# Performance work log

Hardware: AMD Instinct MI355X
Metric: run time of the kernel (lower is better)

## Reference

```python
import jax, jax.numpy as jnp
import numpy as np

DIM = 512
HEADS = 8
HEAD_DIM = DIM // HEADS
HIDDEN = 4 * DIM
EPS = 1e-5


def _ln(x, g, b):
    mu = jnp.mean(x, axis=-1, keepdims=True)
    var = jnp.mean((x - mu) ** 2, axis=-1, keepdims=True)
    return (x - mu) * jax.lax.rsqrt(var + EPS) * g + b


def setup_inputs() -> dict:
    key = jax.random.key(0)
    ks = jax.random.split(key, 12)
    s = lambda fan: 1.0 / np.sqrt(fan)
    return {
        "x": jax.random.normal(ks[0], (2, 4096, DIM), jnp.float32),
        "ln1_g": jnp.ones((DIM,), jnp.float32),
        "ln1_b": jnp.zeros((DIM,), jnp.float32),
        "ln2_g": jnp.ones((DIM,), jnp.float32),
        "ln2_b": jnp.zeros((DIM,), jnp.float32),
        "qkv_w": jax.random.normal(ks[1], (3 * DIM, DIM), jnp.float32) * s(DIM),
        "qkv_b": jnp.zeros((3 * DIM,), jnp.float32),
        "proj_w": jax.random.normal(ks[2], (DIM, DIM), jnp.float32) * s(DIM),
        "proj_b": jnp.zeros((DIM,), jnp.float32),
        "fc1_w": jax.random.normal(ks[3], (HIDDEN, DIM), jnp.float32) * s(DIM),
        "fc1_b": jnp.zeros((HIDDEN,), jnp.float32),
        "fc2_w": jax.random.normal(ks[4], (DIM, HIDDEN), jnp.float32) * s(HIDDEN),
        "fc2_b": jnp.zeros((DIM,), jnp.float32),
    }


def reference(x, ln1_g, ln1_b, ln2_g, ln2_b, qkv_w, qkv_b, proj_w, proj_b,
              fc1_w, fc1_b, fc2_w, fc2_b):
    B, N, C = x.shape
    # --- attention (pre-norm) ---
    h = _ln(x, ln1_g, ln1_b)
    qkv = h @ qkv_w.T + qkv_b                      # [B,N,3C]
    qkv = qkv.reshape(B, N, 3, HEADS, HEAD_DIM)
    q, k, v = (jnp.moveaxis(qkv, 2, 0)[i].transpose(0, 2, 1, 3) for i in range(3))  # [B,H,N,D]
    scale = HEAD_DIM ** -0.5
    attn = jax.nn.softmax(jnp.einsum('bhnd,bhmd->bhnm', q, k) * scale, axis=-1)
    out = jnp.einsum('bhnm,bhmd->bhnd', attn, v)   # [B,H,N,D]
    out = out.transpose(0, 2, 1, 3).reshape(B, N, C)
    x = x + out @ proj_w.T + proj_b
    # --- MLP (pre-norm) ---
    h = _ln(x, ln2_g, ln2_b)
    h = jax.nn.gelu(h @ fc1_w.T + fc1_b, approximate=False)
    return x + h @ fc2_w.T + fc2_b
```

## Files before the change

kernel.cpp:

```cpp
#include <hip/hip_runtime.h>
#include <hip/hip_bf16.h>
#include <hip/hip_fp16.h>
#include <string.h>

using bf16 = __hip_bfloat16;
typedef __attribute__((ext_vector_type(8))) short short8;
typedef __attribute__((ext_vector_type(8))) _Float16 half8;
typedef __attribute__((ext_vector_type(4))) float f32x4;
typedef __attribute__((ext_vector_type(16))) float f32x16;

#define GAS __attribute__((address_space(1)))
#define LAS __attribute__((address_space(3)))

__device__ __forceinline__ void gld_lds16(const void* g, void* l) {
  __builtin_amdgcn_global_load_lds((const GAS void*)g, (LAS void*)l, 16, 0, 0);
}

__device__ __forceinline__ unsigned short f2bfu(float f) {
  bf16 h = __float2bfloat16(f);
  return *reinterpret_cast<unsigned short*>(&h);
}

__device__ __forceinline__ unsigned pack_bf16x2(float lo, float hi) {
  __hip_bfloat162 v = __float22bfloat162_rn(make_float2(lo, hi));
  unsigned u;
  __builtin_memcpy(&u, &v, 4);
  return u;
}

__device__ __forceinline__ unsigned pack_f16x2(float lo, float hi) {
  __half2 v = __float22half2_rn(make_float2(lo, hi));
  unsigned u;
  __builtin_memcpy(&u, &v, 4);
  return u;
}

__global__ __launch_bounds__(256) void cvt_all(const float* __restrict__ w0, bf16* __restrict__ o0,
                                               const float* __restrict__ w1, bf16* __restrict__ o1,
                                               const float* __restrict__ w2, bf16* __restrict__ o2,
                                               const float* __restrict__ w3, bf16* __restrict__ o3) {
  int i = blockIdx.x * 256 + threadIdx.x;
  const float* src; bf16* dst; int off;
  if (i < 196608)      { src = w0; dst = o0; off = i; }
  else if (i < 262144) { src = w1; dst = o1; off = i - 196608; }
  else if (i < 524288) { src = w2; dst = o2; off = i - 262144; }
  else                 { src = w3; dst = o3; off = i - 524288; }
  float4 v = reinterpret_cast<const float4*>(src)[off];
  ushort4 o;
  o.x = f2bfu(v.x); o.y = f2bfu(v.y); o.z = f2bfu(v.z); o.w = f2bfu(v.w);
  reinterpret_cast<ushort4*>(dst)[off] = o;
}

__global__ __launch_bounds__(256) void ln_kernel(const float* __restrict__ x,
                                                 const float* __restrict__ g,
                                                 const float* __restrict__ b,
                                                 bf16* __restrict__ out) {
  const int row = blockIdx.x * 4 + (threadIdx.x >> 6);
  const int lane = threadIdx.x & 63;
  const float4* xr = reinterpret_cast<const float4*>(x + (size_t)row * 512);
  float4 v0 = xr[lane], v1 = xr[64 + lane];
  float s  = v0.x + v0.y + v0.z + v0.w + v1.x + v1.y + v1.z + v1.w;
  float s2 = v0.x*v0.x + v0.y*v0.y + v0.z*v0.z + v0.w*v0.w
           + v1.x*v1.x + v1.y*v1.y + v1.z*v1.z + v1.w*v1.w;
  #pragma unroll
  for (int d = 1; d < 64; d <<= 1) { s += __shfl_xor(s, d); s2 += __shfl_xor(s2, d); }
  const float mu = s * (1.0f / 512.0f);
  const float var = s2 * (1.0f / 512.0f) - mu * mu;
  const float rstd = rsqrtf(var + 1e-5f);
  const float4* g4 = reinterpret_cast<const float4*>(g);
  const float4* b4 = reinterpret_cast<const float4*>(b);
  float4 ga = g4[lane], gb = g4[64 + lane], ba = b4[lane], bb = b4[64 + lane];
  ushort4 o0, o1;
  o0.x = f2bfu((v0.x - mu) * rstd * ga.x + ba.x);
  o0.y = f2bfu((v0.y - mu) * rstd * ga.y + ba.y);
  o0.z = f2bfu((v0.z - mu) * rstd * ga.z + ba.z);
  o0.w = f2bfu((v0.w - mu) * rstd * ga.w + ba.w);
  o1.x = f2bfu((v1.x - mu) * rstd * gb.x + bb.x);
  o1.y = f2bfu((v1.y - mu) * rstd * gb.y + bb.y);
  o1.z = f2bfu((v1.z - mu) * rstd * gb.z + bb.z);
  o1.w = f2bfu((v1.w - mu) * rstd * gb.w + bb.w);
  ushort4* orow = reinterpret_cast<ushort4*>(out + (size_t)row * 512);
  orow[lane] = o0;
  orow[64 + lane] = o1;
}

template <int EPI>
__global__ __launch_bounds__(256) void gemm_bt(const bf16* __restrict__ A,
                                               const bf16* __restrict__ B,
                                               const float* __restrict__ bias,
                                               const float* __restrict__ resid,
                                               void* __restrict__ Cv,
                                               int M, int N, int K) {
  __shared__ bf16 As[128 * 32];
  __shared__ bf16 Bs[128 * 32];
  const int tid = threadIdx.x;
  const int lane = tid & 63, wid = tid >> 6;
  const int lr = lane & 15, lg = lane >> 4;
  const int row0 = blockIdx.x * 128, col0 = blockIdx.y * 128;
  const int wr = (wid >> 1) * 64, wc = (wid & 1) * 64;
  f32x4 acc[4][4] = {};
  const int r1 = tid >> 2,          c1 = (tid & 3) * 8;
  const int r2 = (256 + tid) >> 2,  c2 = ((256 + tid) & 3) * 8;
  for (int kt = 0; kt < K; kt += 32) {
    __syncthreads();
    gld_lds16(A + (size_t)(row0 + r1) * K + kt + c1, As + tid * 8);
    gld_lds16(A + (size_t)(row0 + r2) * K + kt + c2, As + (256 + tid) * 8);
    gld_lds16(B + (size_t)(col0 + r1) * K + kt + c1, Bs + tid * 8);
    gld_lds16(B + (size_t)(col0 + r2) * K + kt + c2, Bs + (256 + tid) * 8);
    __syncthreads();
    short8 af[4], bfr[4];
    #pragma unroll
    for (int mi = 0; mi < 4; ++mi)
      af[mi] = *reinterpret_cast<const short8*>(&As[(wr + mi * 16 + lr) * 32 + lg * 8]);
    #pragma unroll
    for (int nj = 0; nj < 4; ++nj)
      bfr[nj] = *reinterpret_cast<const short8*>(&Bs[(wc + nj * 16 + lr) * 32 + lg * 8]);
    #pragma unroll
    for (int mi = 0; mi < 4; ++mi)
      #pragma unroll
      for (int nj = 0; nj < 4; ++nj)
        acc[mi][nj] = __builtin_amdgcn_mfma_f32_16x16x32_bf16(af[mi], bfr[nj], acc[mi][nj], 0, 0, 0);
  }
  #pragma unroll
  for (int mi = 0; mi < 4; ++mi) {
    #pragma unroll
    for (int nj = 0; nj < 4; ++nj) {
      const int col = col0 + wc + nj * 16 + lr;
      const float bv = bias ? bias[col] : 0.0f;
      #pragma unroll
      for (int rg = 0; rg < 4; ++rg) {
        const int row = row0 + wr + mi * 16 + lg * 4 + rg;
        float v = acc[mi][nj][rg] + bv;
        if constexpr (EPI == 1) v = 0.5f * v * (1.0f + erff(v * 0.70710678118654752f));
        if constexpr (EPI == 2) {
          reinterpret_cast<float*>(Cv)[(size_t)row * N + col] = v + resid[(size_t)row * N + col];
        } else if constexpr (EPI == 3) {
          reinterpret_cast<__half*>(Cv)[(size_t)row * N + col] = __float2half(v);
        } else {
          reinterpret_cast<bf16*>(Cv)[(size_t)row * N + col] = __float2bfloat16(v);
        }
      }
    }
  }
}

template <int EPI>
__global__ __launch_bounds__(256) void gemm_bt64(const bf16* __restrict__ A,
                                                 const bf16* __restrict__ B,
                                                 const float* __restrict__ bias,
                                                 const float* __restrict__ resid,
                                                 void* __restrict__ Cv,
                                                 int M, int N, int K) {
  __shared__ bf16 As[64 * 64];
  __shared__ bf16 Bs[64 * 64];
  const int tid = threadIdx.x;
  const int lane = tid & 63, wid = tid >> 6;
  const int lr = lane & 15, lg = lane >> 4;
  const int row0 = blockIdx.x * 64, col0 = blockIdx.y * 64;
  const int wr = (wid >> 1) * 32, wc = (wid & 1) * 32;
  f32x4 acc[2][2] = {};
  const int xsw = (lr & 7) << 4;
  const int fb0 = lr * 128 + ((lg * 16) ^ xsw);
  const int fb1 = lr * 128 + ((64 + lg * 16) ^ xsw);
  const int ph0 = tid * 16, ph1 = (256 + tid) * 16;
  const int r0 = ph0 >> 7, r1 = ph1 >> 7;
  const int lb0 = ph0 ^ ((r0 & 7) << 4), lb1 = ph1 ^ ((r1 & 7) << 4);
  const char* Ab0 = (const char*)A + (size_t)(row0 + r0) * K * 2 + (lb0 & 127);
  const char* Ab1 = (const char*)A + (size_t)(row0 + r1) * K * 2 + (lb1 & 127);
  const char* Bb0 = (const char*)B + (size_t)(col0 + r0) * K * 2 + (lb0 & 127);
  const char* Bb1 = (const char*)B + (size_t)(col0 + r1) * K * 2 + (lb1 & 127);
  for (int kt = 0; kt < K; kt += 64) {
    __syncthreads();
    gld_lds16(Ab0 + kt * 2, (char*)As + ph0);
    gld_lds16(Ab1 + kt * 2, (char*)As + ph1);
    gld_lds16(Bb0 + kt * 2, (char*)Bs + ph0);
    gld_lds16(Bb1 + kt * 2, (char*)Bs + ph1);
    __syncthreads();
    short8 af0[2], af1[2], bf0[2], bf1[2];
    #pragma unroll
    for (int mi = 0; mi < 2; ++mi) {
      af0[mi] = *reinterpret_cast<const short8*>((const char*)As + (wr + mi * 16) * 128 + fb0);
      af1[mi] = *reinterpret_cast<const short8*>((const char*)As + (wr + mi * 16) * 128 + fb1);
    }
    #pragma unroll
    for (int nj = 0; nj < 2; ++nj) {
      bf0[nj] = *reinterpret_cast<const short8*>((const char*)Bs + (wc + nj * 16) * 128 + fb0);
      bf1[nj] = *reinterpret_cast<const short8*>((const char*)Bs + (wc + nj * 16) * 128 + fb1);
    }
    #pragma unroll
    for (int mi = 0; mi < 2; ++mi)
      #pragma unroll
      for (int nj = 0; nj < 2; ++nj) {
        acc[mi][nj] = __builtin_amdgcn_mfma_f32_16x16x32_bf16(af0[mi], bf0[nj], acc[mi][nj], 0, 0, 0);
        acc[mi][nj] = __builtin_amdgcn_mfma_f32_16x16x32_bf16(af1[mi], bf1[nj], acc[mi][nj], 0, 0, 0);
      }
  }
  #pragma unroll
  for (int mi = 0; mi < 2; ++mi) {
    #pragma unroll
    for (int nj = 0; nj < 2; ++nj) {
      const int col = col0 + wc + nj * 16 + lr;
      const float bv = bias ? bias[col] : 0.0f;
      #pragma unroll
      for (int rg = 0; rg < 4; ++rg) {
        const int row = row0 + wr + mi * 16 + lg * 4 + rg;
        float v = acc[mi][nj][rg] + bv;
        if constexpr (EPI == 1) v = 0.5f * v * (1.0f + erff(v * 0.70710678118654752f));
        if constexpr (EPI == 2) {
          reinterpret_cast<float*>(Cv)[(size_t)row * N + col] = v + resid[(size_t)row * N + col];
        } else {
          reinterpret_cast<bf16*>(Cv)[(size_t)row * N + col] = __float2bfloat16(v);
        }
      }
    }
  }
}

__global__ __launch_bounds__(256) void reshape_qkv(const __half* __restrict__ C,
                                                   __half* __restrict__ q,
                                                   __half* __restrict__ KF,
                                                   __half* __restrict__ VF) {
  const int nt = blockIdx.x;
  const int bh = blockIdx.y;
  const int b = bh >> 3, h = bh & 7;
  __shared__ alignas(16) __half vs[64][72];
  const int tid = threadIdx.x;
  const float qs = 0.125f * 1.44269504088896340736f;
  #pragma unroll
  for (int i = 0; i < 16; ++i) {
    const int idx = i * 256 + tid;
    const int rr = idx >> 6, c = idx & 63;
    const size_t crow = ((size_t)b * 4096 + nt * 64 + rr) * 1536;
    const size_t onb = ((size_t)bh * 4096 + nt * 64 + rr) * 64 + c;
    q[onb] = __float2half(__half2float(C[crow + h * 64 + c]) * qs);
    vs[c][rr] = C[crow + 1024 + h * 64 + c];
  }
  #pragma unroll
  for (int i = 0; i < 2; ++i) {
    const int s = i * 256 + tid;
    const int half_ = s >> 8, dc = (s >> 6) & 3, l = s & 63;
    const int l31 = l & 31, hi2 = l >> 5;
    const __half* src = C + ((size_t)b * 4096 + nt * 64 + half_ * 32 + l31) * 1536
                          + 512 + h * 64 + dc * 16 + hi2 * 8;
    __half* dst = KF + ((size_t)bh * 128 + nt * 2 + half_) * 2048 + dc * 512 + (size_t)l * 8;
    *reinterpret_cast<short8*>(dst) = *reinterpret_cast<const short8*>(src);
  }
  __syncthreads();
  #pragma unroll
  for (int i = 0; i < 2; ++i) {
    const int s = i * 256 + tid;
    const int half_ = (s >> 8) & 1, db = (s >> 7) & 1, c = (s >> 6) & 1, l = s & 63;
    const int d = db * 32 + (l & 31);
    const int n0 = half_ * 32 + c * 16 + ((l >> 5) << 2);
    const short4 lo = *reinterpret_cast<const short4*>(&vs[d][n0]);
    const short4 hi = *reinterpret_cast<const short4*>(&vs[d][n0 + 8]);
    short8 v;
    v[0] = lo.x; v[1] = lo.y; v[2] = lo.z; v[3] = lo.w;
    v[4] = hi.x; v[5] = hi.y; v[6] = hi.z; v[7] = hi.w;
    __half* dst = VF + ((size_t)bh * 128 + nt * 2 + half_) * 2048 + (db * 2 + c) * 512 + (size_t)l * 8;
    *reinterpret_cast<short8*>(dst) = v;
  }
}

__global__ __launch_bounds__(256, 4) void attn_kernel(const __half* __restrict__ Q,
                                                      const __half* __restrict__ KF,
                                                      const __half* __restrict__ VF,
                                                      bf16* __restrict__ Out) {
  const int qt = blockIdx.x;
  const int bh = blockIdx.y;
  const int b = bh >> 3, h = bh & 7;
  __shared__ alignas(16) char smem[17408];
  const int tid = threadIdx.x, w = tid >> 6, lane = tid & 63;
  const int qg = w >> 1, kvh = w & 1;
  const int l31 = lane & 31, hi = lane >> 5;

  const __half* qrow = Q + ((size_t)bh * 4096 + qt * 64 + qg * 32 + l31) * 64 + hi * 8;
  const half8 qf0 = *reinterpret_cast<const half8*>(qrow);
  const half8 qf1 = *reinterpret_cast<const half8*>(qrow + 16);
  const half8 qf2 = *reinterpret_cast<const half8*>(qrow + 32);
  const half8 qf3 = *reinterpret_cast<const half8*>(qrow + 48);

  const char* kfp = (const char*)KF + (size_t)bh * 524288 + (size_t)kvh * 262144 + lane * 16;
  const char* vfp = (const char*)VF + (size_t)bh * 524288 + (size_t)kvh * 262144 + lane * 16;

  f32x16 O0 = {}, O1 = {};
  float mrow = -1e30f, lrow = 0.0f;

  for (int t = 0; t < 64; ++t) {
    const half8 va00 = *reinterpret_cast<const half8*>(vfp);
    const half8 va01 = *reinterpret_cast<const half8*>(vfp + 1024);
    const half8 va10 = *reinterpret_cast<const half8*>(vfp + 2048);
    const half8 va11 = *reinterpret_cast<const half8*>(vfp + 3072);
    vfp += 4096;
    const half8 kf0 = *reinterpret_cast<const half8*>(kfp);
    const half8 kf1 = *reinterpret_cast<const half8*>(kfp + 1024);
    const half8 kf2 = *reinterpret_cast<const half8*>(kfp + 2048);
    const half8 kf3 = *reinterpret_cast<const half8*>(kfp + 3072);
    kfp += 4096;
    f32x16 S = {};
    __builtin_amdgcn_s_setprio(1);
    S = __builtin_amdgcn_mfma_f32_32x32x16_f16(kf0, qf0, S, 0, 0, 0);
    S = __builtin_amdgcn_mfma_f32_32x32x16_f16(kf1, qf1, S, 0, 0, 0);
    S = __builtin_amdgcn_mfma_f32_32x32x16_f16(kf2, qf2, S, 0, 0, 0);
    S = __builtin_amdgcn_mfma_f32_32x32x16_f16(kf3, qf3, S, 0, 0, 0);
    __builtin_amdgcn_s_setprio(0);
    float a0 = fmaxf(fmaxf(S[0], S[1]), fmaxf(S[2], S[3]));
    float a1 = fmaxf(fmaxf(S[4], S[5]), fmaxf(S[6], S[7]));
    float a2 = fmaxf(fmaxf(S[8], S[9]), fmaxf(S[10], S[11]));
    float a3 = fmaxf(fmaxf(S[12], S[13]), fmaxf(S[14], S[15]));
    float rmax = fmaxf(fmaxf(a0, a1), fmaxf(a2, a3));
    float ra = rmax, rb = rmax;
    asm volatile("v_permlane32_swap_b32 %0, %1" : "+v"(ra), "+v"(rb));
    rmax = fmaxf(ra, rb);
    if (!__all(rmax <= mrow + 8.0f)) {
      const float mnew = fmaxf(mrow, rmax);
      const float fsc = __builtin_amdgcn_exp2f(mrow - mnew);
      lrow *= fsc;
      #pragma unroll
      for (int i = 0; i < 16; ++i) { O0[i] *= fsc; O1[i] *= fsc; }
      mrow = mnew;
    }
    #pragma unroll
    for (int i = 0; i < 16; ++i) S[i] = __builtin_amdgcn_exp2f(S[i] - mrow);
    float s0 = (S[0] + S[1]) + (S[2] + S[3]);
    float s1 = (S[4] + S[5]) + (S[6] + S[7]);
    float s2 = (S[8] + S[9]) + (S[10] + S[11]);
    float s3 = (S[12] + S[13]) + (S[14] + S[15]);
    float rsum = (s0 + s1) + (s2 + s3);
    float sa = rsum, sb = rsum;
    asm volatile("v_permlane32_swap_b32 %0, %1" : "+v"(sa), "+v"(sb));
    lrow += sa + sb;
    union U8 { unsigned u[4]; half8 h8; } up0, up1;
    up0.u[0] = pack_f16x2(S[0], S[1]);   up0.u[1] = pack_f16x2(S[2], S[3]);
    up0.u[2] = pack_f16x2(S[4], S[5]);   up0.u[3] = pack_f16x2(S[6], S[7]);
    up1.u[0] = pack_f16x2(S[8], S[9]);   up1.u[1] = pack_f16x2(S[10], S[11]);
    up1.u[2] = pack_f16x2(S[12], S[13]); up1.u[3] = pack_f16x2(S[14], S[15]);
    __builtin_amdgcn_s_setprio(1);
    O0 = __builtin_amdgcn_mfma_f32_32x32x16_f16(va00, up0.h8, O0, 0, 0, 0);
    O0 = __builtin_amdgcn_mfma_f32_32x32x16_f16(va01, up1.h8, O0, 0, 0, 0);
    O1 = __builtin_amdgcn_mfma_f32_32x32x16_f16(va10, up0.h8, O1, 0, 0, 0);
    O1 = __builtin_amdgcn_mfma_f32_32x32x16_f16(va11, up1.h8, O1, 0, 0, 0);
    __builtin_amdgcn_s_setprio(0);
  }

  __syncthreads();
  float* area = reinterpret_cast<float*>(smem) + qg * 2176;
  if (kvh) {
    #pragma unroll
    for (int r = 0; r < 16; ++r) {
      area[r * 64 + lane] = O0[r];
      area[(16 + r) * 64 + lane] = O1[r];
    }
    area[2048 + lane] = mrow;
    area[2112 + lane] = lrow;
  }
  __syncthreads();
  if (!kvh) {
    const float mB = area[2048 + lane], lB = area[2112 + lane];
    const float mx = fmaxf(mrow, mB);
    const float fa = __builtin_amdgcn_exp2f(mrow - mx);
    const float fb = __builtin_amdgcn_exp2f(mB - mx);
    const float inv = 1.0f / (lrow * fa + lB * fb);
    const int qrow2 = qt * 64 + qg * 32 + l31;
    bf16* ob = Out + ((size_t)b * 4096 + qrow2) * 512 + h * 64 + hi * 4;
    #pragma unroll
    for (int db = 0; db < 2; ++db) {
      #pragma unroll
      for (int rq = 0; rq < 4; ++rq) {
        const int r = rq * 4;
        float v0 = ((db ? O1[r + 0] : O0[r + 0]) * fa + area[(db * 16 + r + 0) * 64 + lane] * fb) * inv;
        float v1 = ((db ? O1[r + 1] : O0[r + 1]) * fa + area[(db * 16 + r + 1) * 64 + lane] * fb) * inv;
        float v2 = ((db ? O1[r + 2] : O0[r + 2]) * fa + area[(db * 16 + r + 2) * 64 + lane] * fb) * inv;
        float v3 = ((db ? O1[r + 3] : O0[r + 3]) * fa + area[(db * 16 + r + 3) * 64 + lane] * fb) * inv;
        uint2 st;
        st.x = pack_bf16x2(v0, v1);
        st.y = pack_bf16x2(v2, v3);
        *reinterpret_cast<uint2*>(ob + db * 32 + rq * 8) = st;
      }
    }
  }
}

extern "C" void kernel_launch(void* const* d_in, const int* in_sizes, int n_in,
                              void* d_out, int out_size, void* d_ws, size_t ws_size,
                              hipStream_t stream) {
  const float* x      = (const float*)d_in[0];
  const float* ln1_g  = (const float*)d_in[1];
  const float* ln1_b  = (const float*)d_in[2];
  const float* ln2_g  = (const float*)d_in[3];
  const float* ln2_b  = (const float*)d_in[4];
  const float* qkv_w  = (const float*)d_in[5];
  const float* qkv_b  = (const float*)d_in[6];
  const float* proj_w = (const float*)d_in[7];
  const float* proj_b = (const float*)d_in[8];
  const float* fc1_w  = (const float*)d_in[9];
  const float* fc1_b  = (const float*)d_in[10];
  const float* fc2_w  = (const float*)d_in[11];
  const float* fc2_b  = (const float*)d_in[12];

  char* ws = (char*)d_ws;
  constexpr size_t o_qkvw = 0;
  constexpr size_t o_projw = 1572864;
  constexpr size_t o_fc1w  = 2097152;
  constexpr size_t o_fc2w  = 4194304;
  constexpr size_t o_h     = 6291456;
  constexpr size_t o_qkvC  = 14680064;
  constexpr size_t o_q     = 39845888;
  constexpr size_t o_k     = 48234496;
  constexpr size_t o_vt    = 56623104;
  constexpr size_t o_attn  = 65011712;
  constexpr size_t o_x2    = 73400320;
  constexpr size_t o_fc1o  = o_qkvC;
  constexpr size_t needed  = 90177536;
  if (ws_size < needed) return;

  bf16* qkvw_bf = (bf16*)(ws + o_qkvw);
  bf16* projw_bf = (bf16*)(ws + o_projw);
  bf16* fc1w_bf = (bf16*)(ws + o_fc1w);
  bf16* fc2w_bf = (bf16*)(ws + o_fc2w);
  bf16* h     = (bf16*)(ws + o_h);
  __half* qkvC = (__half*)(ws + o_qkvC);
  __half* q    = (__half*)(ws + o_q);
  __half* kf   = (__half*)(ws + o_k);
  __half* vf   = (__half*)(ws + o_vt);
  bf16* attn  = (bf16*)(ws + o_attn);
  float* x2   = (float*)(ws + o_x2);
  bf16* fc1o  = (bf16*)(ws + o_fc1o);
  float* out  = (float*)d_out;

  cvt_all<<<3072, 256, 0, stream>>>(qkv_w, qkvw_bf, proj_w, projw_bf, fc1_w, fc1w_bf, fc2_w, fc2w_bf);

  ln_kernel<<<2048, 256, 0, stream>>>(x, ln1_g, ln1_b, h);
  gemm_bt<3><<<dim3(64, 12), 256, 0, stream>>>(h, qkvw_bf, qkv_b, nullptr, qkvC, 8192, 1536, 512);
  reshape_qkv<<<dim3(64, 16), 256, 0, stream>>>(qkvC, q, kf, vf);
  attn_kernel<<<dim3(64, 16), 256, 0, stream>>>(q, kf, vf, attn);
  gemm_bt64<2><<<dim3(128, 8), 256, 0, stream>>>(attn, projw_bf, proj_b, x, x2, 8192, 512, 512);
  ln_kernel<<<2048, 256, 0, stream>>>(x2, ln2_g, ln2_b, h);
  gemm_bt<1><<<dim3(64, 16), 256, 0, stream>>>(h, fc1w_bf, fc1_b, nullptr, fc1o, 8192, 2048, 512);
  gemm_bt64<2><<<dim3(128, 8), 256, 0, stream>>>(fc1o, fc2w_bf, fc2_b, x2, out, 8192, 512, 2048);
}
```

Measured before the change: 251.2 us.

## Process two query sub-tiles per wave in attention to reuse K/V fragments

Each wave now computes scores and softmax for two 32-row query blocks against the same K/V fragments. This halves global K/V loads per query row and gives more independent MFMA chains to interleave. The block covers 128 queries, the grid shrinks to 32x16, and launch bounds drop to 2 blocks per CU to allow the doubled accumulator register use. The risks are fewer resident waves to hide load latency and fewer blocks in total.

Result: faster. 238.4 us (-5.1%).

```diff
diff --git a/kernel.cpp b/kernel.cpp
--- a/kernel.cpp
+++ b/kernel.cpp
@@ -262,7 +262,7 @@
   }
 }
 
-__global__ __launch_bounds__(256, 4) void attn_kernel(const __half* __restrict__ Q,
+__global__ __launch_bounds__(256, 2) void attn_kernel(const __half* __restrict__ Q,
                                                       const __half* __restrict__ KF,
                                                       const __half* __restrict__ VF,
                                                       bf16* __restrict__ Out) {
@@ -274,17 +274,20 @@
   const int qg = w >> 1, kvh = w & 1;
   const int l31 = lane & 31, hi = lane >> 5;
 
-  const __half* qrow = Q + ((size_t)bh * 4096 + qt * 64 + qg * 32 + l31) * 64 + hi * 8;
-  const half8 qf0 = *reinterpret_cast<const half8*>(qrow);
-  const half8 qf1 = *reinterpret_cast<const half8*>(qrow + 16);
-  const half8 qf2 = *reinterpret_cast<const half8*>(qrow + 32);
-  const half8 qf3 = *reinterpret_cast<const half8*>(qrow + 48);
+  const __half* qbase = Q + ((size_t)bh * 4096 + qt * 128 + qg * 64 + l31) * 64 + hi * 8;
+  half8 qf0[4], qf1[4];
+  #pragma unroll
+  for (int dc = 0; dc < 4; ++dc) {
+    qf0[dc] = *reinterpret_cast<const half8*>(qbase + dc * 16);
+    qf1[dc] = *reinterpret_cast<const half8*>(qbase + 2048 + dc * 16);
+  }
 
   const char* kfp = (const char*)KF + (size_t)bh * 524288 + (size_t)kvh * 262144 + lane * 16;
   const char* vfp = (const char*)VF + (size_t)bh * 524288 + (size_t)kvh * 262144 + lane * 16;
 
-  f32x16 O0 = {}, O1 = {};
-  float mrow = -1e30f, lrow = 0.0f;
+  f32x16 O00 = {}, O01 = {};
+  f32x16 O10 = {}, O11 = {};
+  float m0 = -1e30f, l0 = 0.0f, m1 = -1e30f, l1 = 0.0f;
 
   for (int t = 0; t < 64; ++t) {
     const half8 va00 = *reinterpret_cast<const half8*>(vfp);
@@ -297,85 +300,134 @@
     const half8 kf2 = *reinterpret_cast<const half8*>(kfp + 2048);
     const half8 kf3 = *reinterpret_cast<const half8*>(kfp + 3072);
     kfp += 4096;
-    f32x16 S = {};
+    f32x16 S0 = {}, S1 = {};
     __builtin_amdgcn_s_setprio(1);
-    S = __builtin_amdgcn_mfma_f32_32x32x16_f16(kf0, qf0, S, 0, 0, 0);
-    S = __builtin_amdgcn_mfma_f32_32x32x16_f16(kf1, qf1, S, 0, 0, 0);
-    S = __builtin_amdgcn_mfma_f32_32x32x16_f16(kf2, qf2, S, 0, 0, 0);
-    S = __builtin_amdgcn_mfma_f32_32x32x16_f16(kf3, qf3, S, 0, 0, 0);
+    S0 = __builtin_amdgcn_mfma_f32_32x32x16_f16(kf0, qf0[0], S0, 0, 0, 0);
+    S1 = __builtin_amdgcn_mfma_f32_32x32x16_f16(kf0, qf1[0], S1, 0, 0, 0);
+    S0 = __builtin_amdgcn_mfma_f32_32x32x16_f16(kf1, qf0[1], S0, 0, 0, 0);
+    S1 = __builtin_amdgcn_mfma_f32_32x32x16_f16(kf1, qf1[1], S1, 0, 0, 0);
+    S0 = __builtin_amdgcn_mfma_f32_32x32x16_f16(kf2, qf0[2], S0, 0, 0, 0);
+    S1 = __builtin_amdgcn_mfma_f32_32x32x16_f16(kf2, qf1[2], S1, 0, 0, 0);
+    S0 = __builtin_amdgcn_mfma_f32_32x32x16_f16(kf3, qf0[3], S0, 0, 0, 0);
+    S1 = __builtin_amdgcn_mfma_f32_32x32x16_f16(kf3, qf1[3], S1, 0, 0, 0);
     __builtin_amdgcn_s_setprio(0);
-    float a0 = fmaxf(fmaxf(S[0], S[1]), fmaxf(S[2], S[3]));
-    float a1 = fmaxf(fmaxf(S[4], S[5]), fmaxf(S[6], S[7]));
-    float a2 = fmaxf(fmaxf(S[8], S[9]), fmaxf(S[10], S[11]));
-    float a3 = fmaxf(fmaxf(S[12], S[13]), fmaxf(S[14], S[15]));
-    float rmax = fmaxf(fmaxf(a0, a1), fmaxf(a2, a3));
-    float ra = rmax, rb = rmax;
-    asm volatile("v_permlane32_swap_b32 %0, %1" : "+v"(ra), "+v"(rb));
-    rmax = fmaxf(ra, rb);
-    if (!__all(rmax <= mrow + 8.0f)) {
-      const float mnew = fmaxf(mrow, rmax);
-      const float fsc = __builtin_amdgcn_exp2f(mrow - mnew);
-      lrow *= fsc;
-      #pragma unroll
-      for (int i = 0; i < 16; ++i) { O0[i] *= fsc; O1[i] *= fsc; }
-      mrow = mnew;
-    }
-    #pragma unroll
-    for (int i = 0; i < 16; ++i) S[i] = __builtin_amdgcn_exp2f(S[i] - mrow);
-    float s0 = (S[0] + S[1]) + (S[2] + S[3]);
-    float s1 = (S[4] + S[5]) + (S[6] + S[7]);
-    float s2 = (S[8] + S[9]) + (S[10] + S[11]);
-    float s3 = (S[12] + S[13]) + (S[14] + S[15]);
-    float rsum = (s0 + s1) + (s2 + s3);
-    float sa = rsum, sb = rsum;
-    asm volatile("v_permlane32_swap_b32 %0, %1" : "+v"(sa), "+v"(sb));
-    lrow += sa + sb;
-    union U8 { unsigned u[4]; half8 h8; } up0, up1;
-    up0.u[0] = pack_f16x2(S[0], S[1]);   up0.u[1] = pack_f16x2(S[2], S[3]);
-    up0.u[2] = pack_f16x2(S[4], S[5]);   up0.u[3] = pack_f16x2(S[6], S[7]);
-    up1.u[0] = pack_f16x2(S[8], S[9]);   up1.u[1] = pack_f16x2(S[10], S[11]);
-    up1.u[2] = pack_f16x2(S[12], S[13]); up1.u[3] = pack_f16x2(S[14], S[15]);
+    union U8 { unsigned u[4]; half8 h8; } p00, p01, p10, p11;
+    {
+      float a0 = fmaxf(fmaxf(S0[0], S0[1]), fmaxf(S0[2], S0[3]));
+      float a1 = fmaxf(fmaxf(S0[4], S0[5]), fmaxf(S0[6], S0[7]));
+      float a2 = fmaxf(fmaxf(S0[8], S0[9]), fmaxf(S0[10], S0[11]));
+      float a3 = fmaxf(fmaxf(S0[12], S0[13]), fmaxf(S0[14], S0[15]));
+      float rmax = fmaxf(fmaxf(a0, a1), fmaxf(a2, a3));
+      float ra = rmax, rb = rmax;
+      asm volatile("v_permlane32_swap_b32 %0, %1" : "+v"(ra), "+v"(rb));
+      rmax = fmaxf(ra, rb);
+      if (!__all(rmax <= m0 + 8.0f)) {
+        const float mnew = fmaxf(m0, rmax);
+        const float fsc = __builtin_amdgcn_exp2f(m0 - mnew);
+        l0 *= fsc;
+        #pragma unroll
+        for (int i = 0; i < 16; ++i) { O00[i] *= fsc; O01[i] *= fsc; }
+        m0 = mnew;
+      }
+      #pragma unroll
+      for (int i = 0; i < 16; ++i) S0[i] = __builtin_amdgcn_exp2f(S0[i] - m0);
+      float s0 = (S0[0] + S0[1]) + (S0[2] + S0[3]);
+      float s1 = (S0[4] + S0[5]) + (S0[6] + S0[7]);
+      float s2 = (S0[8] + S0[9]) + (S0[10] + S0[11]);
+      float s3 = (S0[12] + S0[13]) + (S0[14] + S0[15]);
+      float rsum = (s0 + s1) + (s2 + s3);
+      float sa = rsum, sb = rsum;
+      asm volatile("v_permlane32_swap_b32 %0, %1" : "+v"(sa), "+v"(sb));
+      l0 += sa + sb;
+      p00.u[0] = pack_f16x2(S0[0], S0[1]);   p00.u[1] = pack_f16x2(S0[2], S0[3]);
+      p00.u[2] = pack_f16x2(S0[4], S0[5]);   p00.u[3] = pack_f16x2(S0[6], S0[7]);
+      p01.u[0] = pack_f16x2(S0[8], S0[9]);   p01.u[1] = pack_f16x2(S0[10], S0[11]);
+      p01.u[2] = pack_f16x2(S0[12], S0[13]); p01.u[3] = pack_f16x2(S0[14], S0[15]);
+    }
+    {
+      float a0 = fmaxf(fmaxf(S1[0], S1[1]), fmaxf(S1[2], S1[3]));
+      float a1 = fmaxf(fmaxf(S1[4], S1[5]), fmaxf(S1[6], S1[7]));
+      float a2 = fmaxf(fmaxf(S1[8], S1[9]), fmaxf(S1[10], S1[11]));
+      float a3 = fmaxf(fmaxf(S1[12], S1[13]), fmaxf(S1[14], S1[15]));
+      float rmax = fmaxf(fmaxf(a0, a1), fmaxf(a2, a3));
+      float ra = rmax, rb = rmax;
+      asm volatile("v_permlane32_swap_b32 %0, %1" : "+v"(ra), "+v"(rb));
+      rmax = fmaxf(ra, rb);
+      if (!__all(rmax <= m1 + 8.0f)) {
+        const float mnew = fmaxf(m1, rmax);
+        const float fsc = __builtin_amdgcn_exp2f(m1 - mnew);
+        l1 *= fsc;
+        #pragma unroll
+        for (int i = 0; i < 16; ++i) { O10[i] *= fsc; O11[i] *= fsc; }
+        m1 = mnew;
+      }
+      #pragma unroll
+      for (int i = 0; i < 16; ++i) S1[i] = __builtin_amdgcn_exp2f(S1[i] - m1);
+      float s0 = (S1[0] + S1[1]) + (S1[2] + S1[3]);
+      float s1 = (S1[4] + S1[5]) + (S1[6] + S1[7]);
+      float s2 = (S1[8] + S1[9]) + (S1[10] + S1[11]);
+      float s3 = (S1[12] + S1[13]) + (S1[14] + S1[15]);
+      float rsum = (s0 + s1) + (s2 + s3);
+      float sa = rsum, sb = rsum;
+      asm volatile("v_permlane32_swap_b32 %0, %1" : "+v"(sa), "+v"(sb));
+      l1 += sa + sb;
+      p10.u[0] = pack_f16x2(S1[0], S1[1]);   p10.u[1] = pack_f16x2(S1[2], S1[3]);
+      p10.u[2] = pack_f16x2(S1[4], S1[5]);   p10.u[3] = pack_f16x2(S1[6], S1[7]);
+      p11.u[0] = pack_f16x2(S1[8], S1[9]);   p11.u[1] = pack_f16x2(S1[10], S1[11]);
+      p11.u[2] = pack_f16x2(S1[12], S1[13]); p11.u[3] = pack_f16x2(S1[14], S1[15]);
+    }
     __builtin_amdgcn_s_setprio(1);
-    O0 = __builtin_amdgcn_mfma_f32_32x32x16_f16(va00, up0.h8, O0, 0, 0, 0);
-    O0 = __builtin_amdgcn_mfma_f32_32x32x16_f16(va01, up1.h8, O0, 0, 0, 0);
-    O1 = __builtin_amdgcn_mfma_f32_32x32x16_f16(va10, up0.h8, O1, 0, 0, 0);
-    O1 = __builtin_amdgcn_mfma_f32_32x32x16_f16(va11, up1.h8, O1, 0, 0, 0);
+    O00 = __builtin_amdgcn_mfma_f32_32x32x16_f16(va00, p00.h8, O00, 0, 0, 0);
+    O10 = __builtin_amdgcn_mfma_f32_32x32x16_f16(va00, p10.h8, O10, 0, 0, 0);
+    O00 = __builtin_amdgcn_mfma_f32_32x32x16_f16(va01, p01.h8, O00, 0, 0, 0);
+    O10 = __builtin_amdgcn_mfma_f32_32x32x16_f16(va01, p11.h8, O10, 0, 0, 0);
+    O01 = __builtin_amdgcn_mfma_f32_32x32x16_f16(va10, p00.h8, O01, 0, 0, 0);
+    O11 = __builtin_amdgcn_mfma_f32_32x32x16_f16(va10, p10.h8, O11, 0, 0, 0);
+    O01 = __builtin_amdgcn_mfma_f32_32x32x16_f16(va11, p01.h8, O01, 0, 0, 0);
+    O11 = __builtin_amdgcn_mfma_f32_32x32x16_f16(va11, p11.h8, O11, 0, 0, 0);
     __builtin_amdgcn_s_setprio(0);
   }
 
-  __syncthreads();
   float* area = reinterpret_cast<float*>(smem) + qg * 2176;
-  if (kvh) {
-    #pragma unroll
-    for (int r = 0; r < 16; ++r) {
-      area[r * 64 + lane] = O0[r];
-      area[(16 + r) * 64 + lane] = O1[r];
-    }
-    area[2048 + lane] = mrow;
-    area[2112 + lane] = lrow;
-  }
-  __syncthreads();
-  if (!kvh) {
-    const float mB = area[2048 + lane], lB = area[2112 + lane];
-    const float mx = fmaxf(mrow, mB);
-    const float fa = __builtin_amdgcn_exp2f(mrow - mx);
-    const float fb = __builtin_amdgcn_exp2f(mB - mx);
-    const float inv = 1.0f / (lrow * fa + lB * fb);
-    const int qrow2 = qt * 64 + qg * 32 + l31;
-    bf16* ob = Out + ((size_t)b * 4096 + qrow2) * 512 + h * 64 + hi * 4;
-    #pragma unroll
-    for (int db = 0; db < 2; ++db) {
-      #pragma unroll
-      for (int rq = 0; rq < 4; ++rq) {
-        const int r = rq * 4;
-        float v0 = ((db ? O1[r + 0] : O0[r + 0]) * fa + area[(db * 16 + r + 0) * 64 + lane] * fb) * inv;
-        float v1 = ((db ? O1[r + 1] : O0[r + 1]) * fa + area[(db * 16 + r + 1) * 64 + lane] * fb) * inv;
-        float v2 = ((db ? O1[r + 2] : O0[r + 2]) * fa + area[(db * 16 + r + 2) * 64 + lane] * fb) * inv;
-        float v3 = ((db ? O1[r + 3] : O0[r + 3]) * fa + area[(db * 16 + r + 3) * 64 + lane] * fb) * inv;
-        uint2 st;
-        st.x = pack_bf16x2(v0, v1);
-        st.y = pack_bf16x2(v2, v3);
-        *reinterpret_cast<uint2*>(ob + db * 32 + rq * 8) = st;
+  #pragma unroll
+  for (int qs = 0; qs < 2; ++qs) {
+    const f32x16& Pd0 = qs ? O10 : O00;
+    const f32x16& Pd1 = qs ? O11 : O01;
+    const float mw = qs ? m1 : m0;
+    const float lw = qs ? l1 : l0;
+    __syncthreads();
+    if (kvh) {
+      #pragma unroll
+      for (int r = 0; r < 16; ++r) {
+        area[r * 64 + lane] = Pd0[r];
+        area[(16 + r) * 64 + lane] = Pd1[r];
+      }
+      area[2048 + lane] = mw;
+      area[2112 + lane] = lw;
+    }
+    __syncthreads();
+    if (!kvh) {
+      const float mB = area[2048 + lane], lB = area[2112 + lane];
+      const float mx = fmaxf(mw, mB);
+      const float fa = __builtin_amdgcn_exp2f(mw - mx);
+      const float fb = __builtin_amdgcn_exp2f(mB - mx);
+      const float inv = 1.0f / (lw * fa + lB * fb);
+      const int qrow2 = qt * 128 + qg * 64 + qs * 32 + l31;
+      bf16* ob = Out + ((size_t)b * 4096 + qrow2) * 512 + h * 64 + hi * 4;
+      #pragma unroll
+      for (int db = 0; db < 2; ++db) {
+        #pragma unroll
+        for (int rq = 0; rq < 4; ++rq) {
+          const int r = rq * 4;
+          float v0 = ((db ? Pd1[r + 0] : Pd0[r + 0]) * fa + area[(db * 16 + r + 0) * 64 + lane] * fb) * inv;
+          float v1 = ((db ? Pd1[r + 1] : Pd0[r + 1]) * fa + area[(db * 16 + r + 1) * 64 + lane] * fb) * inv;
+          float v2 = ((db ? Pd1[r + 2] : Pd0[r + 2]) * fa + area[(db * 16 + r + 2) * 64 + lane] * fb) * inv;
+          float v3 = ((db ? Pd1[r + 3] : Pd0[r + 3]) * fa + area[(db * 16 + r + 3) * 64 + lane] * fb) * inv;
+          uint2 st;
+          st.x = pack_bf16x2(v0, v1);
+          st.y = pack_bf16x2(v2, v3);
+          *reinterpret_cast<uint2*>(ob + db * 32 + rq * 8) = st;
+        }
       }
     }
   }
@@ -433,7 +485,7 @@
   ln_kernel<<<2048, 256, 0, stream>>>(x, ln1_g, ln1_b, h);
   gemm_bt<3><<<dim3(64, 12), 256, 0, stream>>>(h, qkvw_bf, qkv_b, nullptr, qkvC, 8192, 1536, 512);
   reshape_qkv<<<dim3(64, 16), 256, 0, stream>>>(qkvC, q, kf, vf);
-  attn_kernel<<<dim3(64, 16), 256, 0, stream>>>(q, kf, vf, attn);
+  attn_kernel<<<dim3(32, 16), 256, 0, stream>>>(q, kf, vf, attn);
   gemm_bt64<2><<<dim3(128, 8), 256, 0, stream>>>(attn, projw_bf, proj_b, x, x2, 8192, 512, 512);
   ln_kernel<<<2048, 256, 0, stream>>>(x2, ln2_g, ln2_b, h);
   gemm_bt<1><<<dim3(64, 16), 256, 0, stream>>>(h, fc1w_bf, fc1_b, nullptr, fc1o, 8192, 2048, 512);
```
